# Optimization experiments

Hardware: AMD Instinct MI355X
Metric: run time of the kernel (lower is better)

## Reference

```python
import jax, jax.numpy as jnp
import numpy as np
import math

D_MODEL, D_K, D_V, H = 512, 64, 64, 8

def setup_inputs() -> dict:
    key = jax.random.key(0)
    ks = jax.random.split(key, 8)
    B, L = 2, 4096
    q = jax.random.normal(ks[0], (B, L, D_MODEL), dtype=jnp.float32)
    k = jax.random.normal(ks[1], (B, L, D_MODEL), dtype=jnp.float32)
    v = jax.random.normal(ks[2], (B, L, D_MODEL), dtype=jnp.float32)
    attention_mask = jnp.ones((B, L), dtype=jnp.int32)
    s = 1.0 / math.sqrt(D_MODEL)
    Wq = jax.random.uniform(ks[3], (D_MODEL, H * D_K), dtype=jnp.float32, minval=-s, maxval=s)
    Wk = jax.random.uniform(ks[4], (D_MODEL, H * D_K), dtype=jnp.float32, minval=-s, maxval=s)
    Wv = jax.random.uniform(ks[5], (D_MODEL, H * D_V), dtype=jnp.float32, minval=-s, maxval=s)
    so = 1.0 / math.sqrt(H * D_V)
    Wo = jax.random.uniform(ks[6], (H * D_V, D_MODEL), dtype=jnp.float32, minval=-so, maxval=so)
    return {"q": q, "k": k, "v": v, "attention_mask": attention_mask,
            "Wq": Wq, "Wk": Wk, "Wv": Wv, "Wo": Wo}

def reference(q, k, v, attention_mask, Wq, Wk, Wv, Wo):
    B, L, _ = q.shape
    scale = 1.0 / math.sqrt(D_K)
    # project and split heads: [B, H, L, d]
    qh = (q @ Wq).reshape(B, L, H, D_K).transpose(0, 2, 1, 3)
    kh = (k @ Wk).reshape(B, L, H, D_K).transpose(0, 2, 1, 3)
    vh = (v @ Wv).reshape(B, L, H, D_V).transpose(0, 2, 1, 3)
    score = jnp.einsum('bhqd,bhkd->bhqk', qh, kh) * scale  # [B,H,L,L]
    mask = attention_mask[:, None, None, :]  # [B,1,1,L]
    score = jnp.where(mask == 0, -jnp.inf, score)
    attn = jax.nn.softmax(score, axis=-1)
    out = jnp.einsum('bhqk,bhkd->bhqd', attn, vh)
    out = out.transpose(0, 2, 1, 3).reshape(B, L, H * D_V)
    return out @ Wo
```

## Files before the change

### kernel.cpp

```cpp
#include <hip/hip_runtime.h>

typedef short bf16x8 __attribute__((ext_vector_type(8)));
typedef float f32x4 __attribute__((ext_vector_type(4)));
typedef unsigned short u16x8 __attribute__((ext_vector_type(8)));

static __device__ __forceinline__ unsigned short f2bf(float f) {
  unsigned int x = __builtin_bit_cast(unsigned int, f);
  x += 0x7FFFu + ((x >> 16) & 1u);
  return (unsigned short)(x >> 16);
}
static __device__ __forceinline__ unsigned int pk2bf(float a, float b) {
  unsigned int ia = __builtin_bit_cast(unsigned int, a) + 0x8000u;
  unsigned int ib = __builtin_bit_cast(unsigned int, b) + 0x8000u;
  return __builtin_amdgcn_perm(ib, ia, 0x07060302u);
}
static __device__ __forceinline__ void gl2lds16(const unsigned short* g, unsigned short* l) {
  __builtin_amdgcn_global_load_lds(
      (const __attribute__((address_space(1))) unsigned int*)g,
      (__attribute__((address_space(3))) unsigned int*)l, 16, 0, 0);
}

__global__ __launch_bounds__(256) void cvt3(const float* __restrict__ q, const float* __restrict__ k,
                                            const float* __restrict__ v,
                                            unsigned short* __restrict__ qo, unsigned short* __restrict__ ko,
                                            unsigned short* __restrict__ vo) {
  const float* src = (blockIdx.y == 0) ? q : (blockIdx.y == 1) ? k : v;
  unsigned short* dst = (blockIdx.y == 0) ? qo : (blockIdx.y == 1) ? ko : vo;
  int i = (blockIdx.x * 256 + threadIdx.x) * 8;
  float4 a = *(const float4*)(src + i);
  float4 b = *(const float4*)(src + i + 4);
  uint4 pk;
  pk.x = pk2bf(a.x, a.y); pk.y = pk2bf(a.z, a.w);
  pk.z = pk2bf(b.x, b.y); pk.w = pk2bf(b.z, b.w);
  *(uint4*)(dst + i) = pk;
}

__global__ __launch_bounds__(256) void wtrans4(const float* __restrict__ Wq, const float* __restrict__ Wk,
                                               const float* __restrict__ Wv, const float* __restrict__ Wo,
                                               unsigned short* __restrict__ WT) {
  __shared__ __align__(16) float T[64 * 68];
  const int z = blockIdx.z;
  const float* W = (z == 0) ? Wq : (z == 1) ? Wk : (z == 2) ? Wv : Wo;
  unsigned short* out = WT + (size_t)z * 512 * 512;
  const int k0 = blockIdx.x * 64, n0 = blockIdx.y * 64;
  const int tid = threadIdx.x;
#pragma unroll
  for (int i = 0; i < 4; ++i) {
    int chunk = i * 256 + tid;
    int row = chunk >> 4, fc = chunk & 15;
    *(float4*)(T + row * 68 + fc * 4) =
        *(const float4*)(W + (size_t)(k0 + row) * 512 + n0 + fc * 4);
  }
  __syncthreads();
#pragma unroll
  for (int i = 0; i < 2; ++i) {
    int chunk = i * 256 + tid;
    int nr = chunk >> 3, kc = chunk & 7;
    u16x8 v;
#pragma unroll
    for (int j = 0; j < 8; ++j) v[j] = f2bf(T[(kc * 8 + j) * 68 + nr]);
    *(u16x8*)(out + (size_t)(n0 + nr) * 512 + k0 + kc * 8) = v;
  }
}

__global__ __launch_bounds__(256) void gemm_qkv(const unsigned short* __restrict__ Aq,
                                                const unsigned short* __restrict__ Ak,
                                                const unsigned short* __restrict__ Av,
                                                const unsigned short* __restrict__ Bt,
                                                unsigned short* __restrict__ C,
                                                float qscale) {
  __shared__ __align__(16) unsigned short Abuf[2][128 * 64];
  __shared__ __align__(16) unsigned short Bbuf[2][64 * 64];
  const int K = 512, LDC = 1536;
  const unsigned short* A = (blockIdx.y < 8) ? Aq : (blockIdx.y < 16) ? Ak : Av;
  const float scale = (blockIdx.y < 8) ? qscale : 1.0f;
  const int tid = threadIdx.x;
  const int wid = tid >> 6, lane = tid & 63, quad = lane >> 4, li = lane & 15;
  const int bm = blockIdx.x * 128, bn = blockIdx.y * 64;
  const int wm = wid * 32;
  const unsigned short* ga[4]; int oa[4];
  const unsigned short* gb[2]; int ob[2];
#pragma unroll
  for (int i = 0; i < 4; ++i) {
    int lam = i * 256 + wid * 64 + lane;
    int r = lam >> 3, c = (lam & 7) ^ (r & 7);
    ga[i] = A + (size_t)(bm + r) * K + c * 8;
    oa[i] = lam * 8;
  }
#pragma unroll
  for (int i = 0; i < 2; ++i) {
    int lam = i * 256 + wid * 64 + lane;
    int r = lam >> 3, c = (lam & 7) ^ (r & 7);
    gb[i] = Bt + (size_t)(bn + r) * K + c * 8;
    ob[i] = lam * 8;
  }
#pragma unroll
  for (int i = 0; i < 4; ++i) { gl2lds16(ga[i], &Abuf[0][oa[i]]); ga[i] += 64; }
#pragma unroll
  for (int i = 0; i < 2; ++i) { gl2lds16(gb[i], &Bbuf[0][ob[i]]); gb[i] += 64; }

  f32x4 acc[2][4] = {};
  const int sw = li & 7;
  for (int s = 0; s < 8; ++s) {
    __syncthreads();
    if (s + 1 < 8) {
      int p = (s + 1) & 1;
#pragma unroll
      for (int i = 0; i < 4; ++i) { gl2lds16(ga[i], &Abuf[p][oa[i]]); ga[i] += 64; }
#pragma unroll
      for (int i = 0; i < 2; ++i) { gl2lds16(gb[i], &Bbuf[p][ob[i]]); gb[i] += 64; }
    }
    const unsigned short* As = &Abuf[s & 1][0];
    const unsigned short* Bs = &Bbuf[s & 1][0];
#pragma unroll
    for (int kk = 0; kk < 2; ++kk) {
      bf16x8 af[2], bfr[4];
#pragma unroll
      for (int t = 0; t < 2; ++t)
        af[t] = *(const bf16x8*)(As + (wm + t * 16 + li) * 64 + (((kk * 4 + quad) ^ sw) * 8));
#pragma unroll
      for (int t = 0; t < 4; ++t)
        bfr[t] = *(const bf16x8*)(Bs + (t * 16 + li) * 64 + (((kk * 4 + quad) ^ sw) * 8));
#pragma unroll
      for (int mt = 0; mt < 2; ++mt)
#pragma unroll
        for (int nt = 0; nt < 4; ++nt)
          acc[mt][nt] = __builtin_amdgcn_mfma_f32_16x16x32_bf16(af[mt], bfr[nt], acc[mt][nt], 0, 0, 0);
    }
  }
#pragma unroll
  for (int mt = 0; mt < 2; ++mt)
#pragma unroll
    for (int nt = 0; nt < 4; ++nt) {
      int r0 = bm + wm + mt * 16 + quad * 4;
      int c  = bn + nt * 16 + li;
#pragma unroll
      for (int r = 0; r < 4; ++r)
        C[(size_t)(r0 + r) * LDC + c] = f2bf(acc[mt][nt][r] * scale);
    }
}

__global__ __launch_bounds__(256) void gemm_o(const unsigned short* __restrict__ A,
                                              const unsigned short* __restrict__ Bt,
                                              float* __restrict__ Cf) {
  __shared__ __align__(16) unsigned short Abuf[2][128 * 64];
  __shared__ __align__(16) unsigned short Bbuf[2][64 * 64];
  const int K = 512, LDC = 512;
  const int tid = threadIdx.x;
  const int wid = tid >> 6, lane = tid & 63, quad = lane >> 4, li = lane & 15;
  const int bm = blockIdx.x * 128, bn = blockIdx.y * 64;
  const int wm = wid * 32;
  const unsigned short* ga[4]; int oa[4];
  const unsigned short* gb[2]; int ob[2];
#pragma unroll
  for (int i = 0; i < 4; ++i) {
    int lam = i * 256 + wid * 64 + lane;
    int r = lam >> 3, c = (lam & 7) ^ (r & 7);
    ga[i] = A + (size_t)(bm + r) * K + c * 8;
    oa[i] = lam * 8;
  }
#pragma unroll
  for (int i = 0; i < 2; ++i) {
    int lam = i * 256 + wid * 64 + lane;
    int r = lam >> 3, c = (lam & 7) ^ (r & 7);
    gb[i] = Bt + (size_t)(bn + r) * K + c * 8;
    ob[i] = lam * 8;
  }
#pragma unroll
  for (int i = 0; i < 4; ++i) { gl2lds16(ga[i], &Abuf[0][oa[i]]); ga[i] += 64; }
#pragma unroll
  for (int i = 0; i < 2; ++i) { gl2lds16(gb[i], &Bbuf[0][ob[i]]); gb[i] += 64; }

  f32x4 acc[2][4] = {};
  const int sw = li & 7;
  for (int s = 0; s < 8; ++s) {
    __syncthreads();
    if (s + 1 < 8) {
      int p = (s + 1) & 1;
#pragma unroll
      for (int i = 0; i < 4; ++i) { gl2lds16(ga[i], &Abuf[p][oa[i]]); ga[i] += 64; }
#pragma unroll
      for (int i = 0; i < 2; ++i) { gl2lds16(gb[i], &Bbuf[p][ob[i]]); gb[i] += 64; }
    }
    const unsigned short* As = &Abuf[s & 1][0];
    const unsigned short* Bs = &Bbuf[s & 1][0];
#pragma unroll
    for (int kk = 0; kk < 2; ++kk) {
      bf16x8 af[2], bfr[4];
#pragma unroll
      for (int t = 0; t < 2; ++t)
        af[t] = *(const bf16x8*)(As + (wm + t * 16 + li) * 64 + (((kk * 4 + quad) ^ sw) * 8));
#pragma unroll
      for (int t = 0; t < 4; ++t)
        bfr[t] = *(const bf16x8*)(Bs + (t * 16 + li) * 64 + (((kk * 4 + quad) ^ sw) * 8));
#pragma unroll
      for (int mt = 0; mt < 2; ++mt)
#pragma unroll
        for (int nt = 0; nt < 4; ++nt)
          acc[mt][nt] = __builtin_amdgcn_mfma_f32_16x16x32_bf16(af[mt], bfr[nt], acc[mt][nt], 0, 0, 0);
    }
  }
#pragma unroll
  for (int mt = 0; mt < 2; ++mt)
#pragma unroll
    for (int nt = 0; nt < 4; ++nt) {
      int r0 = bm + wm + mt * 16 + quad * 4;
      int c  = bn + nt * 16 + li;
#pragma unroll
      for (int r = 0; r < 4; ++r)
        Cf[(size_t)(r0 + r) * LDC + c] = acc[mt][nt][r];
    }
}

__global__ __launch_bounds__(256) void vtrans(const unsigned short* __restrict__ qkv,
                                              unsigned short* __restrict__ vt) {
  __shared__ __align__(16) unsigned short T[64 * 72];
  const int kt = blockIdx.x;
  const int bh = blockIdx.y;
  const int b = bh >> 3, h = bh & 7;
  const int tid = threadIdx.x;
#pragma unroll
  for (int i = 0; i < 2; ++i) {
    int chunk = i * 256 + tid;
    int row = chunk >> 3, c8 = chunk & 7;
    *(uint4*)(T + row * 72 + c8 * 8) =
        *(const uint4*)(qkv + (size_t)(b * 4096 + kt * 64 + row) * 1536 + 1024 + h * 64 + c8 * 8);
  }
  __syncthreads();
#pragma unroll
  for (int i = 0; i < 2; ++i) {
    int chunk = i * 256 + tid;
    int dr = chunk >> 3, c8 = chunk & 7;
    u16x8 v;
#pragma unroll
    for (int j = 0; j < 8; ++j) v[j] = T[(c8 * 8 + j) * 72 + dr];
    *(u16x8*)(vt + (size_t)(bh * 64 + dr) * 4096 + kt * 64 + c8 * 8) = v;
  }
}

__global__ __launch_bounds__(512) void attn(const unsigned short* __restrict__ qkv,
                                            const unsigned short* __restrict__ vt,
                                            const int* __restrict__ mask,
                                            unsigned short* __restrict__ obuf) {
  __shared__ __align__(16) unsigned short Kbuf[2][64 * 64];
  __shared__ __align__(16) unsigned short Vbuf[2][64 * 64];
  __shared__ __align__(16) unsigned short Psh[8][16 * 72];
  __shared__ __align__(16) unsigned short MskBits[256];
  const int qt = blockIdx.x, h = blockIdx.y, b = blockIdx.z;
  const int tid = threadIdx.x;
  const int wid = tid >> 6, lane = tid & 63, quad = lane >> 4, li = lane & 15;
  const size_t tok0 = (size_t)b * 4096;

  if (tid < 256) {
    const int4* mp = (const int4*)(mask + b * 4096 + tid * 16);
    unsigned int bits = 0;
#pragma unroll
    for (int j = 0; j < 4; ++j) {
      int4 m4 = mp[j];
      bits |= (m4.x ? 1u : 0u) << (j * 4 + 0);
      bits |= (m4.y ? 1u : 0u) << (j * 4 + 1);
      bits |= (m4.z ? 1u : 0u) << (j * 4 + 2);
      bits |= (m4.w ? 1u : 0u) << (j * 4 + 3);
    }
    MskBits[tid] = (unsigned short)bits;
  }

  const unsigned short* qp = qkv + (tok0 + qt * 128 + wid * 16 + li) * 1536 + h * 64;
  bf16x8 bq0 = *(const bf16x8*)(qp + quad * 8);
  bf16x8 bq1 = *(const bf16x8*)(qp + 32 + quad * 8);

  const unsigned short* kbase = qkv + tok0 * 1536 + 512 + h * 64;
  const unsigned short* vbase = vt + (size_t)(b * 8 + h) * 64 * 4096;
  const int wk = wid & 3;
  const int lam0 = wk * 128 + lane, lam1 = lam0 + 64;
  const int r0 = lam0 >> 3, c0 = (lam0 & 7) ^ (r0 & 7);
  const int r1 = lam1 >> 3, c1 = (lam1 & 7) ^ (r1 & 7);
  const unsigned short *g0, *g1;
  size_t kstride;
  unsigned short *lb0, *lb1;
  if (wid < 4) {
    g0 = kbase + (size_t)r0 * 1536 + c0 * 8;
    g1 = kbase + (size_t)r1 * 1536 + c1 * 8;
    kstride = (size_t)64 * 1536;
    lb0 = &Kbuf[0][0]; lb1 = &Kbuf[1][0];
  } else {
    g0 = vbase + (size_t)r0 * 4096 + c0 * 8;
    g1 = vbase + (size_t)r1 * 4096 + c1 * 8;
    kstride = 64;
    lb0 = &Vbuf[0][0]; lb1 = &Vbuf[1][0];
  }
  const int o0 = lam0 * 8, o1 = lam1 * 8;

  gl2lds16(g0, lb0 + o0);
  gl2lds16(g1, lb0 + o1);
  g0 += kstride; g1 += kstride;

  f32x4 lacc = {};
  f32x4 accO[4] = {};
  unsigned short* Pw = &Psh[wid][0];
  const int sw = li & 7;

  for (int t = 0; t < 64; ++t) {
    __syncthreads();
    if (t < 63) {
      unsigned short* lb = ((t + 1) & 1) ? lb1 : lb0;
      gl2lds16(g0, lb + o0);
      gl2lds16(g1, lb + o1);
      g0 += kstride; g1 += kstride;
    }
    const unsigned short* Ks = &Kbuf[t & 1][0];
    const unsigned short* Vs = &Vbuf[t & 1][0];

    f32x4 s[4];
#pragma unroll
    for (int kb = 0; kb < 4; ++kb) {
      const unsigned short* kr = Ks + (kb * 16 + li) * 64;
      bf16x8 ak0 = *(const bf16x8*)(kr + ((quad ^ sw) * 8));
      bf16x8 ak1 = *(const bf16x8*)(kr + (((4 + quad) ^ sw) * 8));
      f32x4 z = {};
      z = __builtin_amdgcn_mfma_f32_16x16x32_bf16(ak0, bq0, z, 0, 0, 0);
      z = __builtin_amdgcn_mfma_f32_16x16x32_bf16(ak1, bq1, z, 0, 0, 0);
      s[kb] = z;
    }
    unsigned long long mbits = *(const unsigned long long*)(MskBits + t * 4);
    if (mbits != ~0ull) {
#pragma unroll
      for (int kb = 0; kb < 4; ++kb)
#pragma unroll
        for (int r = 0; r < 4; ++r) {
          int key = kb * 16 + quad * 4 + r;
          if (!((mbits >> key) & 1ull)) s[kb][r] = -1e30f;
        }
    }
#pragma unroll
    for (int kb = 0; kb < 4; ++kb) {
#pragma unroll
      for (int r = 0; r < 4; ++r) s[kb][r] = __builtin_amdgcn_exp2f(s[kb][r]);
      lacc += s[kb];
      uint2 pk;
      pk.x = pk2bf(s[kb][0], s[kb][1]);
      pk.y = pk2bf(s[kb][2], s[kb][3]);
      *(uint2*)(Pw + li * 72 + kb * 16 + quad * 4) = pk;
    }
    bf16x8 p0 = *(const bf16x8*)(Pw + li * 72 + quad * 8);
    bf16x8 p1 = *(const bf16x8*)(Pw + li * 72 + 32 + quad * 8);
#pragma unroll
    for (int dc = 0; dc < 4; ++dc) {
      const unsigned short* vr = Vs + (dc * 16 + li) * 64;
      bf16x8 bv0 = *(const bf16x8*)(vr + ((quad ^ sw) * 8));
      bf16x8 bv1 = *(const bf16x8*)(vr + (((4 + quad) ^ sw) * 8));
      accO[dc] = __builtin_amdgcn_mfma_f32_16x16x32_bf16(p0, bv0, accO[dc], 0, 0, 0);
      accO[dc] = __builtin_amdgcn_mfma_f32_16x16x32_bf16(p1, bv1, accO[dc], 0, 0, 0);
    }
  }
  float lt = lacc[0] + lacc[1] + lacc[2] + lacc[3];
  lt += __shfl_xor(lt, 16);
  lt += __shfl_xor(lt, 32);
  float lv0 = 1.f / __shfl(lt, quad * 4 + 0);
  float lv1 = 1.f / __shfl(lt, quad * 4 + 1);
  float lv2 = 1.f / __shfl(lt, quad * 4 + 2);
  float lv3 = 1.f / __shfl(lt, quad * 4 + 3);
#pragma unroll
  for (int dc = 0; dc < 4; ++dc) {
    size_t r0q = tok0 + qt * 128 + wid * 16 + quad * 4;
    size_t col = h * 64 + dc * 16 + li;
    obuf[(r0q + 0) * 512 + col] = f2bf(accO[dc][0] * lv0);
    obuf[(r0q + 1) * 512 + col] = f2bf(accO[dc][1] * lv1);
    obuf[(r0q + 2) * 512 + col] = f2bf(accO[dc][2] * lv2);
    obuf[(r0q + 3) * 512 + col] = f2bf(accO[dc][3] * lv3);
  }
}

extern "C" void kernel_launch(void* const* d_in, const int* in_sizes, int n_in,
                              void* d_out, int out_size, void* d_ws, size_t ws_size,
                              hipStream_t stream) {
  const float* q  = (const float*)d_in[0];
  const float* k  = (const float*)d_in[1];
  const float* v  = (const float*)d_in[2];
  const int* mask = (const int*)d_in[3];
  const float* Wq = (const float*)d_in[4];
  const float* Wk = (const float*)d_in[5];
  const float* Wv = (const float*)d_in[6];
  const float* Wo = (const float*)d_in[7];
  float* out = (float*)d_out;

  char* ws = (char*)d_ws;
  const size_t SA = (size_t)8192 * 512 * 2;
  unsigned short* qbf  = (unsigned short*)(ws);
  unsigned short* kbf  = (unsigned short*)(ws + SA);
  unsigned short* vbf  = (unsigned short*)(ws + 2 * SA);
  unsigned short* qkvh = (unsigned short*)(ws + 3 * SA);
  unsigned short* wAll = (unsigned short*)(ws + 6 * SA);
  unsigned short* woT  = wAll + (size_t)3 * 512 * 512;
  unsigned short* vtb  = qbf;
  unsigned short* ob   = kbf;

  dim3 cg(2048, 3);
  cvt3<<<cg, 256, 0, stream>>>(q, k, v, qbf, kbf, vbf);
  dim3 wg(8, 8, 4);
  wtrans4<<<wg, 256, 0, stream>>>(Wq, Wk, Wv, Wo, wAll);
  const float qscale = 0.125f * 1.44269504f;
  dim3 gq(64, 24);
  gemm_qkv<<<gq, 256, 0, stream>>>(qbf, kbf, vbf, wAll, qkvh, qscale);
  dim3 vg(64, 16);
  vtrans<<<vg, 256, 0, stream>>>(qkvh, vtb);
  dim3 ag(32, 8, 2);
  attn<<<ag, 512, 0, stream>>>(qkvh, vtb, mask, ob);
  dim3 go(64, 8);
  gemm_o<<<go, 256, 0, stream>>>(ob, woT, out);
}
```

Before: 226.9 us.

## Split attention over key halves, add combine kernel, enlarge QKV GEMM tiles

The attention kernel now splits the key range into two halves across blockIdx.z. That doubles the grid to 512 workgroups, which should fill more of the CUs. Each half writes unnormalized fp32 partial outputs and row sums to workspace, and a new combine kernel sums the halves and normalizes. This is valid without max tracking because the kernel already uses a fixed-offset exp2. The row sum is now computed with an MFMA against a ones vector instead of vector adds. Separately, the inputs are packed into one interleaved [8192,1536] bf16 buffer and the QKV GEMM uses 128x128 tiles with K-step 32, raising arithmetic intensity. The trade-off is extra fp32 partial-output traffic and one more kernel launch.

```diff
diff --git a/kernel.cpp b/kernel.cpp
--- a/kernel.cpp
+++ b/kernel.cpp
@@ -22,17 +22,17 @@
 
 __global__ __launch_bounds__(256) void cvt3(const float* __restrict__ q, const float* __restrict__ k,
                                             const float* __restrict__ v,
-                                            unsigned short* __restrict__ qo, unsigned short* __restrict__ ko,
-                                            unsigned short* __restrict__ vo) {
-  const float* src = (blockIdx.y == 0) ? q : (blockIdx.y == 1) ? k : v;
-  unsigned short* dst = (blockIdx.y == 0) ? qo : (blockIdx.y == 1) ? ko : vo;
+                                            unsigned short* __restrict__ xbf) {
+  const int sec = blockIdx.y;
+  const float* src = (sec == 0) ? q : (sec == 1) ? k : v;
   int i = (blockIdx.x * 256 + threadIdx.x) * 8;
+  int row = i >> 9, col = i & 511;
   float4 a = *(const float4*)(src + i);
   float4 b = *(const float4*)(src + i + 4);
   uint4 pk;
   pk.x = pk2bf(a.x, a.y); pk.y = pk2bf(a.z, a.w);
   pk.z = pk2bf(b.x, b.y); pk.w = pk2bf(b.z, b.w);
-  *(uint4*)(dst + i) = pk;
+  *(uint4*)(xbf + (size_t)row * 1536 + sec * 512 + col) = pk;
 }
 
 __global__ __launch_bounds__(256) void wtrans4(const float* __restrict__ Wq, const float* __restrict__ Wk,
@@ -63,80 +63,70 @@
   }
 }
 
-__global__ __launch_bounds__(256) void gemm_qkv(const unsigned short* __restrict__ Aq,
-                                                const unsigned short* __restrict__ Ak,
-                                                const unsigned short* __restrict__ Av,
+__global__ __launch_bounds__(256) void gemm_qkv(const unsigned short* __restrict__ xbf,
                                                 const unsigned short* __restrict__ Bt,
                                                 unsigned short* __restrict__ C,
                                                 float qscale) {
-  __shared__ __align__(16) unsigned short Abuf[2][128 * 64];
-  __shared__ __align__(16) unsigned short Bbuf[2][64 * 64];
-  const int K = 512, LDC = 1536;
-  const unsigned short* A = (blockIdx.y < 8) ? Aq : (blockIdx.y < 16) ? Ak : Av;
-  const float scale = (blockIdx.y < 8) ? qscale : 1.0f;
+  __shared__ __align__(16) unsigned short Abuf[2][128 * 32];
+  __shared__ __align__(16) unsigned short Bbuf[2][128 * 32];
+  const int by = blockIdx.y;
+  const unsigned short* A = xbf + (by >> 2) * 512;
+  const float scale = (by < 4) ? qscale : 1.0f;
   const int tid = threadIdx.x;
   const int wid = tid >> 6, lane = tid & 63, quad = lane >> 4, li = lane & 15;
-  const int bm = blockIdx.x * 128, bn = blockIdx.y * 64;
-  const int wm = wid * 32;
-  const unsigned short* ga[4]; int oa[4];
-  const unsigned short* gb[2]; int ob[2];
-#pragma unroll
-  for (int i = 0; i < 4; ++i) {
-    int lam = i * 256 + wid * 64 + lane;
-    int r = lam >> 3, c = (lam & 7) ^ (r & 7);
-    ga[i] = A + (size_t)(bm + r) * K + c * 8;
+  const int bm = blockIdx.x * 128, bn = by * 128;
+  const int wm = (wid & 1) * 64, wn = (wid >> 1) * 64;
+  const unsigned short* ga[2]; int oa[2];
+  const unsigned short* gb[2]; int obx[2];
+#pragma unroll
+  for (int i = 0; i < 2; ++i) {
+    int lam = i * 256 + tid;
+    int r = lam >> 2, c = (lam & 3) ^ (r & 3);
+    ga[i] = A + (size_t)(bm + r) * 1536 + c * 8;
     oa[i] = lam * 8;
-  }
-#pragma unroll
-  for (int i = 0; i < 2; ++i) {
-    int lam = i * 256 + wid * 64 + lane;
-    int r = lam >> 3, c = (lam & 7) ^ (r & 7);
-    gb[i] = Bt + (size_t)(bn + r) * K + c * 8;
-    ob[i] = lam * 8;
-  }
-#pragma unroll
-  for (int i = 0; i < 4; ++i) { gl2lds16(ga[i], &Abuf[0][oa[i]]); ga[i] += 64; }
-#pragma unroll
-  for (int i = 0; i < 2; ++i) { gl2lds16(gb[i], &Bbuf[0][ob[i]]); gb[i] += 64; }
-
-  f32x4 acc[2][4] = {};
-  const int sw = li & 7;
-  for (int s = 0; s < 8; ++s) {
+    gb[i] = Bt + (size_t)(bn + r) * 512 + c * 8;
+    obx[i] = lam * 8;
+  }
+#pragma unroll
+  for (int i = 0; i < 2; ++i) {
+    gl2lds16(ga[i], &Abuf[0][oa[i]]); ga[i] += 32;
+    gl2lds16(gb[i], &Bbuf[0][obx[i]]); gb[i] += 32;
+  }
+  f32x4 acc[4][4] = {};
+  const int sw = li & 3;
+  for (int s = 0; s < 16; ++s) {
     __syncthreads();
-    if (s + 1 < 8) {
+    if (s + 1 < 16) {
       int p = (s + 1) & 1;
 #pragma unroll
-      for (int i = 0; i < 4; ++i) { gl2lds16(ga[i], &Abuf[p][oa[i]]); ga[i] += 64; }
-#pragma unroll
-      for (int i = 0; i < 2; ++i) { gl2lds16(gb[i], &Bbuf[p][ob[i]]); gb[i] += 64; }
+      for (int i = 0; i < 2; ++i) {
+        gl2lds16(ga[i], &Abuf[p][oa[i]]); ga[i] += 32;
+        gl2lds16(gb[i], &Bbuf[p][obx[i]]); gb[i] += 32;
+      }
     }
     const unsigned short* As = &Abuf[s & 1][0];
     const unsigned short* Bs = &Bbuf[s & 1][0];
-#pragma unroll
-    for (int kk = 0; kk < 2; ++kk) {
-      bf16x8 af[2], bfr[4];
-#pragma unroll
-      for (int t = 0; t < 2; ++t)
-        af[t] = *(const bf16x8*)(As + (wm + t * 16 + li) * 64 + (((kk * 4 + quad) ^ sw) * 8));
-#pragma unroll
-      for (int t = 0; t < 4; ++t)
-        bfr[t] = *(const bf16x8*)(Bs + (t * 16 + li) * 64 + (((kk * 4 + quad) ^ sw) * 8));
-#pragma unroll
-      for (int mt = 0; mt < 2; ++mt)
-#pragma unroll
-        for (int nt = 0; nt < 4; ++nt)
-          acc[mt][nt] = __builtin_amdgcn_mfma_f32_16x16x32_bf16(af[mt], bfr[nt], acc[mt][nt], 0, 0, 0);
-    }
-  }
-#pragma unroll
-  for (int mt = 0; mt < 2; ++mt)
+    bf16x8 af[4], bfr[4];
+#pragma unroll
+    for (int t = 0; t < 4; ++t) {
+      af[t]  = *(const bf16x8*)(As + (wm + t * 16 + li) * 32 + ((quad ^ sw) * 8));
+      bfr[t] = *(const bf16x8*)(Bs + (wn + t * 16 + li) * 32 + ((quad ^ sw) * 8));
+    }
+#pragma unroll
+    for (int mt = 0; mt < 4; ++mt)
+#pragma unroll
+      for (int nt = 0; nt < 4; ++nt)
+        acc[mt][nt] = __builtin_amdgcn_mfma_f32_16x16x32_bf16(af[mt], bfr[nt], acc[mt][nt], 0, 0, 0);
+  }
+#pragma unroll
+  for (int mt = 0; mt < 4; ++mt)
 #pragma unroll
     for (int nt = 0; nt < 4; ++nt) {
       int r0 = bm + wm + mt * 16 + quad * 4;
-      int c  = bn + nt * 16 + li;
+      int c  = bn + wn + nt * 16 + li;
 #pragma unroll
       for (int r = 0; r < 4; ++r)
-        C[(size_t)(r0 + r) * LDC + c] = f2bf(acc[mt][nt][r] * scale);
+        C[(size_t)(r0 + r) * 1536 + c] = f2bf(acc[mt][nt][r] * scale);
     }
 }
 
@@ -241,12 +231,15 @@
 __global__ __launch_bounds__(512) void attn(const unsigned short* __restrict__ qkv,
                                             const unsigned short* __restrict__ vt,
                                             const int* __restrict__ mask,
-                                            unsigned short* __restrict__ obuf) {
+                                            float* __restrict__ O0, float* __restrict__ O1,
+                                            float* __restrict__ Lb) {
   __shared__ __align__(16) unsigned short Kbuf[2][64 * 64];
   __shared__ __align__(16) unsigned short Vbuf[2][64 * 64];
   __shared__ __align__(16) unsigned short Psh[8][16 * 72];
   __shared__ __align__(16) unsigned short MskBits[256];
-  const int qt = blockIdx.x, h = blockIdx.y, b = blockIdx.z;
+  const int qt = blockIdx.x, h = blockIdx.y, z = blockIdx.z;
+  const int b = z >> 1, half = z & 1;
+  const int t0 = half * 32;
   const int tid = threadIdx.x;
   const int wid = tid >> 6, lane = tid & 63, quad = lane >> 4, li = lane & 15;
   const size_t tok0 = (size_t)b * 4096;
@@ -279,13 +272,13 @@
   size_t kstride;
   unsigned short *lb0, *lb1;
   if (wid < 4) {
-    g0 = kbase + (size_t)r0 * 1536 + c0 * 8;
-    g1 = kbase + (size_t)r1 * 1536 + c1 * 8;
+    g0 = kbase + (size_t)(t0 * 64 + r0) * 1536 + c0 * 8;
+    g1 = kbase + (size_t)(t0 * 64 + r1) * 1536 + c1 * 8;
     kstride = (size_t)64 * 1536;
     lb0 = &Kbuf[0][0]; lb1 = &Kbuf[1][0];
   } else {
-    g0 = vbase + (size_t)r0 * 4096 + c0 * 8;
-    g1 = vbase + (size_t)r1 * 4096 + c1 * 8;
+    g0 = vbase + (size_t)r0 * 4096 + t0 * 64 + c0 * 8;
+    g1 = vbase + (size_t)r1 * 4096 + t0 * 64 + c1 * 8;
     kstride = 64;
     lb0 = &Vbuf[0][0]; lb1 = &Vbuf[1][0];
   }
@@ -295,21 +288,25 @@
   gl2lds16(g1, lb0 + o1);
   g0 += kstride; g1 += kstride;
 
-  f32x4 lacc = {};
   f32x4 accO[4] = {};
+  f32x4 accL = {};
+  bf16x8 bones;
+#pragma unroll
+  for (int j = 0; j < 8; ++j) bones[j] = (short)0x3F80;
   unsigned short* Pw = &Psh[wid][0];
   const int sw = li & 7;
 
-  for (int t = 0; t < 64; ++t) {
+  for (int tt = 0; tt < 32; ++tt) {
+    const int t = t0 + tt;
     __syncthreads();
-    if (t < 63) {
-      unsigned short* lb = ((t + 1) & 1) ? lb1 : lb0;
+    if (tt < 31) {
+      unsigned short* lb = ((tt + 1) & 1) ? lb1 : lb0;
       gl2lds16(g0, lb + o0);
       gl2lds16(g1, lb + o1);
       g0 += kstride; g1 += kstride;
     }
-    const unsigned short* Ks = &Kbuf[t & 1][0];
-    const unsigned short* Vs = &Vbuf[t & 1][0];
+    const unsigned short* Ks = &Kbuf[tt & 1][0];
+    const unsigned short* Vs = &Vbuf[tt & 1][0];
 
     f32x4 s[4];
 #pragma unroll
@@ -317,10 +314,10 @@
       const unsigned short* kr = Ks + (kb * 16 + li) * 64;
       bf16x8 ak0 = *(const bf16x8*)(kr + ((quad ^ sw) * 8));
       bf16x8 ak1 = *(const bf16x8*)(kr + (((4 + quad) ^ sw) * 8));
-      f32x4 z = {};
-      z = __builtin_amdgcn_mfma_f32_16x16x32_bf16(ak0, bq0, z, 0, 0, 0);
-      z = __builtin_amdgcn_mfma_f32_16x16x32_bf16(ak1, bq1, z, 0, 0, 0);
-      s[kb] = z;
+      f32x4 zv = {};
+      zv = __builtin_amdgcn_mfma_f32_16x16x32_bf16(ak0, bq0, zv, 0, 0, 0);
+      zv = __builtin_amdgcn_mfma_f32_16x16x32_bf16(ak1, bq1, zv, 0, 0, 0);
+      s[kb] = zv;
     }
     unsigned long long mbits = *(const unsigned long long*)(MskBits + t * 4);
     if (mbits != ~0ull) {
@@ -336,7 +333,6 @@
     for (int kb = 0; kb < 4; ++kb) {
 #pragma unroll
       for (int r = 0; r < 4; ++r) s[kb][r] = __builtin_amdgcn_exp2f(s[kb][r]);
-      lacc += s[kb];
       uint2 pk;
       pk.x = pk2bf(s[kb][0], s[kb][1]);
       pk.y = pk2bf(s[kb][2], s[kb][3]);
@@ -352,23 +348,37 @@
       accO[dc] = __builtin_amdgcn_mfma_f32_16x16x32_bf16(p0, bv0, accO[dc], 0, 0, 0);
       accO[dc] = __builtin_amdgcn_mfma_f32_16x16x32_bf16(p1, bv1, accO[dc], 0, 0, 0);
     }
-  }
-  float lt = lacc[0] + lacc[1] + lacc[2] + lacc[3];
-  lt += __shfl_xor(lt, 16);
-  lt += __shfl_xor(lt, 32);
-  float lv0 = 1.f / __shfl(lt, quad * 4 + 0);
-  float lv1 = 1.f / __shfl(lt, quad * 4 + 1);
-  float lv2 = 1.f / __shfl(lt, quad * 4 + 2);
-  float lv3 = 1.f / __shfl(lt, quad * 4 + 3);
+    accL = __builtin_amdgcn_mfma_f32_16x16x32_bf16(p0, bones, accL, 0, 0, 0);
+    accL = __builtin_amdgcn_mfma_f32_16x16x32_bf16(p1, bones, accL, 0, 0, 0);
+  }
+  float* Oh = half ? O1 : O0;
+  const size_t rq = tok0 + qt * 128 + wid * 16 + quad * 4;
 #pragma unroll
   for (int dc = 0; dc < 4; ++dc) {
-    size_t r0q = tok0 + qt * 128 + wid * 16 + quad * 4;
     size_t col = h * 64 + dc * 16 + li;
-    obuf[(r0q + 0) * 512 + col] = f2bf(accO[dc][0] * lv0);
-    obuf[(r0q + 1) * 512 + col] = f2bf(accO[dc][1] * lv1);
-    obuf[(r0q + 2) * 512 + col] = f2bf(accO[dc][2] * lv2);
-    obuf[(r0q + 3) * 512 + col] = f2bf(accO[dc][3] * lv3);
-  }
+#pragma unroll
+    for (int r = 0; r < 4; ++r)
+      Oh[(rq + r) * 512 + col] = accO[dc][r];
+  }
+  if (li == 0) {
+#pragma unroll
+    for (int r = 0; r < 4; ++r)
+      Lb[((size_t)half * 8192 + rq + r) * 8 + h] = accL[r];
+  }
+}
+
+__global__ __launch_bounds__(256) void cmb(const float* __restrict__ O0, const float* __restrict__ O1,
+                                           const float* __restrict__ Lb,
+                                           unsigned short* __restrict__ ob) {
+  int idx = (blockIdx.x * 256 + threadIdx.x) * 4;
+  int tok = idx >> 9, h = (idx >> 6) & 7;
+  float inv = 1.f / (Lb[(size_t)tok * 8 + h] + Lb[(size_t)(8192 + tok) * 8 + h]);
+  float4 a = *(const float4*)(O0 + idx);
+  float4 b = *(const float4*)(O1 + idx);
+  uint2 pk;
+  pk.x = pk2bf((a.x + b.x) * inv, (a.y + b.y) * inv);
+  pk.y = pk2bf((a.z + b.z) * inv, (a.w + b.w) * inv);
+  *(uint2*)(ob + idx) = pk;
 }
 
 extern "C" void kernel_launch(void* const* d_in, const int* in_sizes, int n_in,
@@ -385,27 +395,29 @@
   float* out = (float*)d_out;
 
   char* ws = (char*)d_ws;
-  const size_t SA = (size_t)8192 * 512 * 2;
-  unsigned short* qbf  = (unsigned short*)(ws);
-  unsigned short* kbf  = (unsigned short*)(ws + SA);
-  unsigned short* vbf  = (unsigned short*)(ws + 2 * SA);
-  unsigned short* qkvh = (unsigned short*)(ws + 3 * SA);
-  unsigned short* wAll = (unsigned short*)(ws + 6 * SA);
+  const size_t MB = 1024 * 1024;
+  unsigned short* xbf  = (unsigned short*)(ws);
+  unsigned short* vtb  = (unsigned short*)(ws + 16 * MB);
+  unsigned short* obb  = (unsigned short*)(ws + 16 * MB);
+  unsigned short* qkvh = (unsigned short*)(ws + 24 * MB);
+  unsigned short* wAll = (unsigned short*)(ws + 48 * MB);
   unsigned short* woT  = wAll + (size_t)3 * 512 * 512;
-  unsigned short* vtb  = qbf;
-  unsigned short* ob   = kbf;
+  float* O0f = (float*)(ws);
+  float* O1f = (float*)(ws + 50 * MB);
+  float* Lb  = (float*)(ws + 66 * MB);
 
   dim3 cg(2048, 3);
-  cvt3<<<cg, 256, 0, stream>>>(q, k, v, qbf, kbf, vbf);
+  cvt3<<<cg, 256, 0, stream>>>(q, k, v, xbf);
   dim3 wg(8, 8, 4);
   wtrans4<<<wg, 256, 0, stream>>>(Wq, Wk, Wv, Wo, wAll);
   const float qscale = 0.125f * 1.44269504f;
-  dim3 gq(64, 24);
-  gemm_qkv<<<gq, 256, 0, stream>>>(qbf, kbf, vbf, wAll, qkvh, qscale);
+  dim3 gq(64, 12);
+  gemm_qkv<<<gq, 256, 0, stream>>>(xbf, wAll, qkvh, qscale);
   dim3 vg(64, 16);
   vtrans<<<vg, 256, 0, stream>>>(qkvh, vtb);
-  dim3 ag(32, 8, 2);
-  attn<<<ag, 512, 0, stream>>>(qkvh, vtb, mask, ob);
+  dim3 ag(32, 8, 4);
+  attn<<<ag, 512, 0, stream>>>(qkvh, vtb, mask, O0f, O1f, Lb);
+  cmb<<<4096, 256, 0, stream>>>(O0f, O1f, Lb, obb);
   dim3 go(64, 8);
-  gemm_o<<<go, 256, 0, stream>>>(ob, woT, out);
-}
+  gemm_o<<<go, 256, 0, stream>>>(obb, woT, out);
+}
```

Result: slower. 235.1 us (+3.6%).
